# Performance work log

Measured on AMD Instinct MI355X. Metric: run time of the kernel, lower is better.

Reference implementation:

```python
import jax, jax.numpy as jnp
import numpy as np

N = 50000      # nodes
E = 600000     # edges
D_IN = 128     # node_dim
D = 128        # out_channels
T = 4          # num_node_types
R = 4          # num_edge_types
L = 2          # num_layers
C = 8          # num_class
G = 512        # graphs in batch


def setup_inputs() -> dict:
    key = jax.random.key(0)
    ks = jax.random.split(key, 12)
    s = 0.05
    x = jax.random.normal(ks[0], (N, D_IN), jnp.float32)
    node_type = jax.random.randint(ks[1], (N,), 0, T)
    edge_index = jax.random.randint(ks[2], (2, E), 0, N)
    edge_type = jax.random.randint(ks[3], (E,), 0, R)
    batch = jnp.sort(jax.random.randint(ks[4], (N,), 0, G))
    # learned params
    W_het = jax.random.normal(ks[5], (T, D_IN, D), jnp.float32) * s
    b_het = jnp.zeros((T, D), jnp.float32)
    conv_W = jax.random.normal(ks[6], (L, R, D, D), jnp.float32) * s
    conv_b = jnp.zeros((L, R, D), jnp.float32)
    fuse_W = jax.random.normal(ks[7], (R * D, D), jnp.float32) * s
    fuse_b = jnp.zeros((D,), jnp.float32)
    cls_W = jax.random.normal(ks[8], (D, C), jnp.float32) * s
    cls_b = jnp.zeros((C,), jnp.float32)
    return dict(x=x, W_het=W_het, b_het=b_het, conv_W=conv_W, conv_b=conv_b,
                fuse_W=fuse_W, fuse_b=fuse_b, cls_W=cls_W, cls_b=cls_b,
                node_type=node_type, edge_index=edge_index, edge_type=edge_type,
                batch=batch)


def reference(x, W_het, b_het, conv_W, conv_b, fuse_W, fuse_b, cls_W, cls_b,
              node_type, edge_index, edge_type, batch):
    n = x.shape[0]
    # HeteroLinear: per-node-type linear. Compute all T projections then select.
    x_all = jnp.einsum('nd,tdo->tno', x, W_het)          # [T, N, D]
    h = x_all[node_type, jnp.arange(n)] + b_het[node_type]
    src, dst = edge_index[0], edge_index[1]
    for l in range(L):
        hs = h[src]                                       # [E, D] gather once per layer
        outs = []
        for r in range(R):
            # edges of relation r only (boolean mask == per-relation edge filtering)
            m = hs @ conv_W[l, r]                         # [E, D]
            m = m * (edge_type == r).astype(m.dtype)[:, None]
            agg = jax.ops.segment_sum(m, dst, num_segments=n)  # scatter-add to dst
            outs.append(agg + conv_b[l, r])
        h = jax.nn.relu(jnp.concatenate(outs, axis=1) @ fuse_W + fuse_b)
    # global mean pool over graphs
    counts = jax.ops.segment_sum(jnp.ones((n,), h.dtype), batch, num_segments=G)
    emb = jax.ops.segment_sum(h, batch, num_segments=G) / jnp.maximum(counts, 1.0)[:, None]
    logits = emb @ cls_W + cls_b
    return emb, logits
```

## Files before the change

kernel.cpp:

```cpp
#include <hip/hip_runtime.h>

#define N_NODES 50000
#define N_EDGES 600000
#define DIM     128
#define RR      4
#define LL      2
#define GG      512
#define CC      8
#define NB_SCAN ((N_NODES + 255) / 256)
#define EC      (N_EDGES / 4)
#define FB      ((EC + 255) / 256)
#define TB      ((N_NODES + 255) / 256)
#define NBH     ((N_NODES + 63) / 64)
#define CB      (1026 + 3125)

typedef short bf16x8 __attribute__((ext_vector_type(8)));
typedef float f32x4  __attribute__((ext_vector_type(4)));

__device__ __forceinline__ float bf16_to_f(unsigned short u) {
    return __uint_as_float(((unsigned int)u) << 16);
}
__device__ __forceinline__ unsigned short f_to_bf16(float f) {
    unsigned int u = __float_as_uint(f);
    u += 0x7FFFu + ((u >> 16) & 1u);
    return (unsigned short)(u >> 16);
}
__device__ __forceinline__ float loadf(const void* p, long i, int isbf) {
    if (isbf) return bf16_to_f(((const unsigned short*)p)[i]);
    return ((const float*)p)[i];
}
__device__ __forceinline__ void storef(void* p, long i, float v, int isbf) {
    if (isbf) ((unsigned short*)p)[i] = f_to_bf16(v);
    else      ((float*)p)[i] = v;
}

__global__ void cg_init(const unsigned int* __restrict__ xw, int* __restrict__ flag,
                        int* __restrict__ deg_tb) {
    __shared__ int cnt;
    int tid = threadIdx.x;
    int t = blockIdx.x * 256 + tid;
    if (t < N_NODES + 16) deg_tb[t] = 0;
    if (blockIdx.x == 0) {
        if (tid == 0) cnt = 0;
        __syncthreads();
        unsigned int w = xw[tid];
        unsigned int e = (w >> 7) & 0xFFu;
        atomicAdd(&cnt, (e >= 110u && e <= 133u) ? 1 : 0);
        __syncthreads();
        if (tid == 0) *flag = (cnt >= 128) ? 1 : 0;
    }
}

__global__ void cg_hist_canon(const int* __restrict__ edge_index, const int* __restrict__ node_type,
                              int* __restrict__ deg, int* __restrict__ tb,
                              const void* __restrict__ x,
                              const void* __restrict__ W_het, const void* __restrict__ b_het,
                              const void* __restrict__ conv_W, const void* __restrict__ fuse_W,
                              const void* __restrict__ conv_b, const void* __restrict__ fuse_b,
                              const int* __restrict__ flagp,
                              unsigned short* __restrict__ xb, unsigned short* __restrict__ Wt,
                              float* __restrict__ bhf,
                              unsigned short* __restrict__ M2t, float* __restrict__ cvec) {
    __shared__ float s[256];
    int bk = blockIdx.x;
    int tid = threadIdx.x;
    if (bk < FB) {
        __shared__ int loc[4];
        if (tid < 4) loc[tid] = 0;
        __syncthreads();
        int t = bk * 256 + tid;
        if (t < EC) {
            int d0 = edge_index[N_EDGES + t];
            int d1 = edge_index[N_EDGES + t + EC];
            int d2 = edge_index[N_EDGES + t + 2 * EC];
            int d3 = edge_index[N_EDGES + t + 3 * EC];
            atomicAdd(&deg[d0], 1);
            atomicAdd(&deg[d1], 1);
            atomicAdd(&deg[d2], 1);
            atomicAdd(&deg[d3], 1);
        }
        if (t < N_NODES) atomicAdd(&loc[node_type[t]], 1);
        __syncthreads();
        if (tid < 4 && loc[tid]) atomicAdd(&tb[tid], loc[tid]);
        return;
    }
    int b = bk - FB;
    int isbf = *flagp;
    if (b < 512) {
        int lr = b >> 6;
        int d  = (b & 63) * 2 + (tid >> 7);
        int r  = lr & 3;
        int o  = tid & 127;
        float acc = 0.0f;
        for (int k = 0; k < DIM; k++) {
            acc += loadf(conv_W, (long)(lr * DIM + d) * DIM + k, isbf)
                 * loadf(fuse_W, (long)(r * DIM + k) * DIM + o, isbf);
        }
        M2t[((long)lr * DIM + o) * DIM + d] = f_to_bf16(acc);
    } else if (b < 768) {
        int bc = b - 512;
        int l  = bc >> 7;
        int o  = bc & 127;
        float part = 0.0f;
        for (int rk = tid; rk < RR * DIM; rk += 256) {
            part += loadf(conv_b, (long)l * RR * DIM + rk, isbf)
                  * loadf(fuse_W, (long)rk * DIM + o, isbf);
        }
        s[tid] = part;
        __syncthreads();
        for (int off = 128; off > 0; off >>= 1) {
            if (tid < off) s[tid] += s[tid + off];
            __syncthreads();
        }
        if (tid == 0) cvec[bc] = s[0] + loadf(fuse_b, o, isbf);
    } else if (b < 1024) {
        int pair = (b - 768) * 2 + (tid >> 7);
        int t = pair >> 7;
        int o = pair & 127;
        int d = tid & 127;
        float v = loadf(W_het, ((long)t * DIM + d) * DIM + o, isbf);
        Wt[((long)t * DIM + o) * DIM + d] = f_to_bf16(v);
    } else if (b < 1026) {
        int idx = (b - 1024) * 256 + tid;
        if (idx < 4 * DIM) bhf[idx] = loadf(b_het, idx, isbf);
    } else {
        long i = ((long)(b - 1026) * 256 + tid) * 8;
        if (i >= (long)N_NODES * DIM) return;
        if (isbf) {
            *(uint4*)(xb + i) = *(const uint4*)((const unsigned short*)x + i);
        } else {
            const float* xf = (const float*)x + i;
            float4 f0 = *(const float4*)xf;
            float4 f1 = *(const float4*)(xf + 4);
            uint4 o;
            o.x = (unsigned int)f_to_bf16(f0.x) | ((unsigned int)f_to_bf16(f0.y) << 16);
            o.y = (unsigned int)f_to_bf16(f0.z) | ((unsigned int)f_to_bf16(f0.w) << 16);
            o.z = (unsigned int)f_to_bf16(f1.x) | ((unsigned int)f_to_bf16(f1.y) << 16);
            o.w = (unsigned int)f_to_bf16(f1.z) | ((unsigned int)f_to_bf16(f1.w) << 16);
            *(uint4*)(xb + i) = o;
        }
    }
}

__global__ void cg_scan_a(const int* __restrict__ deg, int* __restrict__ blocksum) {
    __shared__ int s[256];
    int tid = threadIdx.x;
    int i = blockIdx.x * 256 + tid;
    s[tid] = (i < N_NODES) ? deg[i] : 0;
    __syncthreads();
    for (int off = 128; off > 0; off >>= 1) {
        if (tid < off) s[tid] += s[tid + off];
        __syncthreads();
    }
    if (tid == 0) blocksum[blockIdx.x] = s[0];
}

__global__ void cg_scan_b(const int* __restrict__ blocksum, int* __restrict__ blockoff,
                          int* __restrict__ rowptr, int* __restrict__ tb) {
    __shared__ int s[256];
    int tid = threadIdx.x;
    int v = (tid < NB_SCAN) ? blocksum[tid] : 0;
    s[tid] = v;
    __syncthreads();
    for (int off = 1; off < 256; off <<= 1) {
        int a = (tid >= off) ? s[tid - off] : 0;
        __syncthreads();
        s[tid] += a;
        __syncthreads();
    }
    if (tid < NB_SCAN) blockoff[tid] = s[tid] - v;
    if (tid == 255) rowptr[N_NODES] = s[255];
    if (tid == 0) {
        int run = 0;
        for (int t = 0; t < 4; t++) {
            tb[8 + t] = run;
            tb[4 + t] = run;
            run += tb[t];
        }
        tb[12] = run;
    }
}

__global__ void cg_scan_tfill(const int* __restrict__ deg, const int* __restrict__ blockoff,
                              int* __restrict__ rowptr, int* __restrict__ cursor,
                              const int* __restrict__ node_type, int* __restrict__ tb,
                              int* __restrict__ tlist) {
    int bk = blockIdx.x;
    int tid = threadIdx.x;
    if (bk < NB_SCAN) {
        __shared__ int s[256];
        int i = bk * 256 + tid;
        int v = (i < N_NODES) ? deg[i] : 0;
        s[tid] = v;
        __syncthreads();
        for (int off = 1; off < 256; off <<= 1) {
            int a = (tid >= off) ? s[tid - off] : 0;
            __syncthreads();
            s[tid] += a;
            __syncthreads();
        }
        if (i < N_NODES) {
            int val = blockoff[bk] + s[tid] - v;
            rowptr[i] = val;
            cursor[i] = val;
        }
    } else {
        __shared__ int lcur[4];
        __shared__ int lbase[4];
        if (tid < 4) lcur[tid] = 0;
        __syncthreads();
        int n = (bk - NB_SCAN) * 256 + tid;
        int slot = -1, t = 0;
        if (n < N_NODES) {
            t = node_type[n];
            slot = atomicAdd(&lcur[t], 1);
        }
        __syncthreads();
        if (tid < 4) lbase[tid] = atomicAdd(&tb[4 + tid], lcur[tid]);
        __syncthreads();
        if (n < N_NODES) tlist[lbase[t] + slot] = n;
    }
}

#define APAD 136

__global__ void cg_fill_hetero(const int* __restrict__ edge_index, const int* __restrict__ edge_type,
                               int* __restrict__ cursor, int* __restrict__ eidx,
                               const unsigned short* __restrict__ xb,
                               const unsigned short* __restrict__ Wt,
                               const float* __restrict__ bhf,
                               const int* __restrict__ tlist, const int* __restrict__ tb,
                               unsigned short* __restrict__ h) {
    __shared__ unsigned short a_lds[64][APAD];
    __shared__ unsigned short b_lds[DIM][APAD];
    int bk = blockIdx.x;
    int tx = threadIdx.x;
    if (bk < FB) {
        int t = bk * 256 + tx;
        if (t >= EC) return;
#pragma unroll
        for (int k = 0; k < 4; k++) {
            int e = t + k * EC;
            int d = edge_index[N_EDGES + e];
            int pos = atomicAdd(&cursor[d], 1);
            eidx[pos] = (edge_index[e] << 2) | edge_type[e];
        }
        return;
    }
    int bb = bk - FB;
    int t    = bb / NBH;
    int nblk = bb - t * NBH;
    int rows_base = tb[8 + t] + nblk * 64;
    int rend = tb[8 + t + 1];
    if (rows_base >= rend) return;
    const unsigned short* Wsrc = Wt + (long)t * DIM * DIM;
    for (int i = tx; i < 2048; i += 256) {
        uint4 w = *(const uint4*)(Wsrc + i * 8);
        int o = i >> 4, d = (i & 15) * 8;
        *(uint4*)&b_lds[o][d] = w;
    }
    for (int i = tx; i < 1024; i += 256) {
        int row = i >> 4, seg = (i & 15) * 8;
        int gr = rows_base + row;
        uint4 w = make_uint4(0u, 0u, 0u, 0u);
        if (gr < rend) {
            int n = tlist[gr];
            w = *(const uint4*)(xb + (long)n * DIM + seg);
        }
        *(uint4*)&a_lds[row][seg] = w;
    }
    __syncthreads();
    int wv = tx >> 6, lane = tx & 63;
    int m16 = lane & 15, quad = lane >> 4;
    f32x4 acc[8];
#pragma unroll
    for (int c = 0; c < 8; c++) acc[c] = (f32x4){0.f, 0.f, 0.f, 0.f};
    for (int ks = 0; ks < 4; ks++) {
        int koff = ks * 32 + quad * 8;
        bf16x8 af = *(const bf16x8*)(const void*)&a_lds[wv * 16 + m16][koff];
#pragma unroll
        for (int c = 0; c < 8; c++) {
            bf16x8 bfr = *(const bf16x8*)(const void*)&b_lds[c * 16 + m16][koff];
            acc[c] = __builtin_amdgcn_mfma_f32_16x16x32_bf16(af, bfr, acc[c], 0, 0, 0);
        }
    }
    __syncthreads();
#pragma unroll
    for (int c = 0; c < 8; c++) {
#pragma unroll
        for (int i = 0; i < 4; i++) {
            int row = wv * 16 + quad * 4 + i;
            int col = c * 16 + m16;
            a_lds[row][col] = f_to_bf16(acc[c][i] + bhf[t * DIM + col]);
        }
    }
    __syncthreads();
    for (int i = tx; i < 1024; i += 256) {
        int row = i >> 4, seg = (i & 15) * 8;
        int gr = rows_base + row;
        if (gr < rend) {
            int n = tlist[gr];
            *(uint4*)(h + (long)n * DIM + seg) = *(const uint4*)&a_lds[row][seg];
        }
    }
}

__global__ void cg_pgemm_mfma(const unsigned short* __restrict__ h,
                              const unsigned short* __restrict__ M2t, int l,
                              unsigned short* __restrict__ P) {
    int r  = blockIdx.y;
    int n0 = blockIdx.x * 64;
    __shared__ unsigned short a_lds[64][APAD];
    __shared__ unsigned short b_lds[DIM][APAD];
    int tx = threadIdx.x;
    const unsigned short* Bsrc = M2t + (long)(l * RR + r) * DIM * DIM;
    for (int i = tx; i < 2048; i += 256) {
        uint4 w = *(const uint4*)(Bsrc + i * 8);
        int o = i >> 4, d = (i & 15) * 8;
        *(uint4*)&b_lds[o][d] = w;
    }
    for (int i = tx; i < 1024; i += 256) {
        int row = i >> 4, seg = (i & 15) * 8;
        int n = n0 + row;
        uint4 w = make_uint4(0u, 0u, 0u, 0u);
        if (n < N_NODES) w = *(const uint4*)(h + (long)n * DIM + seg);
        *(uint4*)&a_lds[row][seg] = w;
    }
    __syncthreads();
    int wv = tx >> 6, lane = tx & 63;
    int m16 = lane & 15, quad = lane >> 4;
    f32x4 acc[8];
#pragma unroll
    for (int c = 0; c < 8; c++) acc[c] = (f32x4){0.f, 0.f, 0.f, 0.f};
    for (int ks = 0; ks < 4; ks++) {
        int koff = ks * 32 + quad * 8;
        bf16x8 af = *(const bf16x8*)(const void*)&a_lds[wv * 16 + m16][koff];
#pragma unroll
        for (int c = 0; c < 8; c++) {
            bf16x8 bfr = *(const bf16x8*)(const void*)&b_lds[c * 16 + m16][koff];
            acc[c] = __builtin_amdgcn_mfma_f32_16x16x32_bf16(af, bfr, acc[c], 0, 0, 0);
        }
    }
    __syncthreads();
#pragma unroll
    for (int c = 0; c < 8; c++) {
#pragma unroll
        for (int i = 0; i < 4; i++) {
            int row = wv * 16 + quad * 4 + i;
            int col = c * 16 + m16;
            a_lds[row][col] = f_to_bf16(acc[c][i]);
        }
    }
    __syncthreads();
    for (int i = tx; i < 1024; i += 256) {
        int row = i >> 4, seg = (i & 15) * 8;
        int n = n0 + row;
        if (n < N_NODES)
            *(uint4*)(P + (long)n * (RR * DIM) + r * DIM + seg) = *(const uint4*)&a_lds[row][seg];
    }
}

__global__ void cg_gather4(const unsigned short* __restrict__ P, const int* __restrict__ rowptr,
                           const int* __restrict__ eidx, const float* __restrict__ cv,
                           unsigned short* __restrict__ hout) {
    int wid  = (blockIdx.x * 256 + threadIdx.x) >> 6;
    int lane = threadIdx.x & 63;
    if (wid >= N_NODES) return;
    int eg = lane >> 4;
    int ol = lane & 15;
    int start = rowptr[wid];
    int end   = rowptr[wid + 1];
    float a[8] = {0.f, 0.f, 0.f, 0.f, 0.f, 0.f, 0.f, 0.f};
    int j = start + eg;
    for (; j + 4 < end; j += 8) {
        int v0 = eidx[j];
        int v1 = eidx[j + 4];
        const uint4 w0 = *(const uint4*)(P + (long)(v0 >> 2) * (RR * DIM) + (v0 & 3) * DIM + ol * 8);
        const uint4 w1 = *(const uint4*)(P + (long)(v1 >> 2) * (RR * DIM) + (v1 & 3) * DIM + ol * 8);
        a[0] += bf16_to_f((unsigned short)(w0.x & 0xFFFFu)) + bf16_to_f((unsigned short)(w1.x & 0xFFFFu));
        a[1] += bf16_to_f((unsigned short)(w0.x >> 16))     + bf16_to_f((unsigned short)(w1.x >> 16));
        a[2] += bf16_to_f((unsigned short)(w0.y & 0xFFFFu)) + bf16_to_f((unsigned short)(w1.y & 0xFFFFu));
        a[3] += bf16_to_f((unsigned short)(w0.y >> 16))     + bf16_to_f((unsigned short)(w1.y >> 16));
        a[4] += bf16_to_f((unsigned short)(w0.z & 0xFFFFu)) + bf16_to_f((unsigned short)(w1.z & 0xFFFFu));
        a[5] += bf16_to_f((unsigned short)(w0.z >> 16))     + bf16_to_f((unsigned short)(w1.z >> 16));
        a[6] += bf16_to_f((unsigned short)(w0.w & 0xFFFFu)) + bf16_to_f((unsigned short)(w1.w & 0xFFFFu));
        a[7] += bf16_to_f((unsigned short)(w0.w >> 16))     + bf16_to_f((unsigned short)(w1.w >> 16));
    }
    if (j < end) {
        int v = eidx[j];
        const uint4 w = *(const uint4*)(P + (long)(v >> 2) * (RR * DIM) + (v & 3) * DIM + ol * 8);
        a[0] += bf16_to_f((unsigned short)(w.x & 0xFFFFu));
        a[1] += bf16_to_f((unsigned short)(w.x >> 16));
        a[2] += bf16_to_f((unsigned short)(w.y & 0xFFFFu));
        a[3] += bf16_to_f((unsigned short)(w.y >> 16));
        a[4] += bf16_to_f((unsigned short)(w.z & 0xFFFFu));
        a[5] += bf16_to_f((unsigned short)(w.z >> 16));
        a[6] += bf16_to_f((unsigned short)(w.w & 0xFFFFu));
        a[7] += bf16_to_f((unsigned short)(w.w >> 16));
    }
#pragma unroll
    for (int i = 0; i < 8; i++) {
        a[i] += __shfl_xor(a[i], 16);
        a[i] += __shfl_xor(a[i], 32);
    }
    if (eg == 0) {
        int o0 = ol * 8;
        float v[8];
#pragma unroll
        for (int i = 0; i < 8; i++) {
            float s = a[i] + cv[o0 + i];
            v[i] = s > 0.0f ? s : 0.0f;
        }
        uint4 o4;
        o4.x = (unsigned int)f_to_bf16(v[0]) | ((unsigned int)f_to_bf16(v[1]) << 16);
        o4.y = (unsigned int)f_to_bf16(v[2]) | ((unsigned int)f_to_bf16(v[3]) << 16);
        o4.z = (unsigned int)f_to_bf16(v[4]) | ((unsigned int)f_to_bf16(v[5]) << 16);
        o4.w = (unsigned int)f_to_bf16(v[6]) | ((unsigned int)f_to_bf16(v[7]) << 16);
        *(uint4*)(hout + (long)wid * DIM + o0) = o4;
    }
}

__global__ void cg_pool_logits(const unsigned short* __restrict__ h, const int* __restrict__ batch,
                               const void* __restrict__ cls_W, const void* __restrict__ cls_b,
                               const int* __restrict__ flagp, void* __restrict__ out) {
    __shared__ float acc_s[4][DIM];
    __shared__ float emb_s[DIM];
    int g   = blockIdx.x;
    int tid = threadIdx.x;
    int wv  = tid >> 6;
    int lane = tid & 63;
    int sub = lane >> 4;
    int ol  = lane & 15;
    int isbf = *flagp;
    int lo = 0, hi = N_NODES;
    while (lo < hi) { int mid = (lo + hi) >> 1; if (batch[mid] < g) lo = mid + 1; else hi = mid; }
    int start = lo;
    hi = N_NODES;
    while (lo < hi) { int mid = (lo + hi) >> 1; if (batch[mid] < g + 1) lo = mid + 1; else hi = mid; }
    int end = lo;
    float a[8] = {0.f, 0.f, 0.f, 0.f, 0.f, 0.f, 0.f, 0.f};
    for (int n = start + wv * 4 + sub; n < end; n += 16) {
        uint4 w = *(const uint4*)(h + (long)n * DIM + ol * 8);
        a[0] += bf16_to_f((unsigned short)(w.x & 0xFFFFu));
        a[1] += bf16_to_f((unsigned short)(w.x >> 16));
        a[2] += bf16_to_f((unsigned short)(w.y & 0xFFFFu));
        a[3] += bf16_to_f((unsigned short)(w.y >> 16));
        a[4] += bf16_to_f((unsigned short)(w.z & 0xFFFFu));
        a[5] += bf16_to_f((unsigned short)(w.z >> 16));
        a[6] += bf16_to_f((unsigned short)(w.w & 0xFFFFu));
        a[7] += bf16_to_f((unsigned short)(w.w >> 16));
    }
#pragma unroll
    for (int i = 0; i < 8; i++) {
        a[i] += __shfl_xor(a[i], 16);
        a[i] += __shfl_xor(a[i], 32);
    }
    if (sub == 0) {
#pragma unroll
        for (int i = 0; i < 8; i++) acc_s[wv][ol * 8 + i] = a[i];
    }
    __syncthreads();
    int cnt = end - start;
    float inv = 1.0f / (float)(cnt > 1 ? cnt : 1);
    if (tid < DIM) {
        float e = (acc_s[0][tid] + acc_s[1][tid] + acc_s[2][tid] + acc_s[3][tid]) * inv;
        emb_s[tid] = e;
        storef(out, (long)g * DIM + tid, e, isbf);
    }
    __syncthreads();
    if (tid < 128) {
        int c  = tid >> 4;
        int kk = tid & 15;
        float p = 0.0f;
#pragma unroll
        for (int k = kk * 8; k < kk * 8 + 8; k++)
            p += emb_s[k] * loadf(cls_W, (long)k * CC + c, isbf);
        p += __shfl_xor(p, 1);
        p += __shfl_xor(p, 2);
        p += __shfl_xor(p, 4);
        p += __shfl_xor(p, 8);
        if (kk == 0)
            storef(out, (long)GG * DIM + g * CC + c, p + loadf(cls_b, c, isbf), isbf);
    }
}

extern "C" void kernel_launch(void* const* d_in, const int* in_sizes, int n_in,
                              void* d_out, int out_size, void* d_ws, size_t ws_size,
                              hipStream_t stream) {
    const void* x      = d_in[0];
    const void* W_het  = d_in[1];
    const void* b_het  = d_in[2];
    const void* conv_W = d_in[3];
    const void* conv_b = d_in[4];
    const void* fuse_W = d_in[5];
    const void* fuse_b = d_in[6];
    const void* cls_W  = d_in[7];
    const void* cls_b  = d_in[8];
    const int* node_type  = (const int*)d_in[9];
    const int* edge_index = (const int*)d_in[10];
    const int* edge_type  = (const int*)d_in[11];
    const int* batch      = (const int*)d_in[12];

    char* base = (char*)d_ws;
    unsigned short* hbf      = (unsigned short*)(base + 0);
    unsigned short* P        = (unsigned short*)(base + 12800000);
    unsigned short* xb       = (unsigned short*)(base + 64000000);
    unsigned short* Wt       = (unsigned short*)(base + 76800000);
    float*          bhf      = (float*)(base + 76931072);
    unsigned short* M2t      = (unsigned short*)(base + 76933120);
    float*          cvec     = (float*)(base + 77195264);
    int*            rowptr   = (int*)(base + 77196288);
    int*            cursor   = (int*)(base + 77396320);
    int*            deg      = (int*)(base + 77596352);
    int*            tb       = (int*)(base + 77796352);
    int*            blocksum = (int*)(base + 77796416);
    int*            blockoff = (int*)(base + 77797440);
    int*            eidx     = (int*)(base + 77798464);
    int*            tlist    = (int*)(base + 80198464);
    int*            flag     = (int*)(base + 80398464);

    cg_init<<<(N_NODES + 16 + 255) / 256, 256, 0, stream>>>((const unsigned int*)x, flag, deg);
    cg_hist_canon<<<FB + CB, 256, 0, stream>>>(edge_index, node_type, deg, tb,
                                               x, W_het, b_het, conv_W, fuse_W,
                                               conv_b, fuse_b, flag,
                                               xb, Wt, bhf, M2t, cvec);
    cg_scan_a<<<NB_SCAN, 256, 0, stream>>>(deg, blocksum);
    cg_scan_b<<<1, 256, 0, stream>>>(blocksum, blockoff, rowptr, tb);
    cg_scan_tfill<<<NB_SCAN + TB, 256, 0, stream>>>(deg, blockoff, rowptr, cursor,
                                                    node_type, tb, tlist);
    cg_fill_hetero<<<FB + 4 * NBH, 256, 0, stream>>>(edge_index, edge_type, cursor, eidx,
                                                     xb, Wt, bhf, tlist, tb, hbf);

    for (int l = 0; l < LL; l++) {
        cg_pgemm_mfma<<<dim3(NBH, RR), 256, 0, stream>>>(hbf, M2t, l, P);
        cg_gather4<<<(N_NODES * 64 + 255) / 256, 256, 0, stream>>>(
            P, rowptr, eidx, cvec + l * DIM, hbf);
    }

    cg_pool_logits<<<GG, 256, 0, stream>>>(hbf, batch, cls_W, cls_b, flag, d_out);
}
```

Before: 317.6 us.

## Build CSR with two-pass block-bucketed sort and fuse second pass with layer-0 GEMM

Replaces the per-edge global atomic scatter into CSR with a two-pass counting sort. Pass one buckets edges by 256-node destination block using LDS histograms and one global atomic per bucket, writing (payload, dst) pairs to a temp buffer. Pass two does the per-node scatter using LDS atomics and runs in the same launch as the layer-0 projection GEMM. This removes one launch and cuts global atomic contention and scattered writes, at the cost of an extra temp buffer pass and more kernel complexity.

```diff
diff --git a/kernel.cpp b/kernel.cpp
--- a/kernel.cpp
+++ b/kernel.cpp
@@ -156,6 +156,7 @@
 }
 
 __global__ void cg_scan_b(const int* __restrict__ blocksum, int* __restrict__ blockoff,
+                          int* __restrict__ ccursor,
                           int* __restrict__ rowptr, int* __restrict__ tb) {
     __shared__ int s[256];
     int tid = threadIdx.x;
@@ -168,7 +169,11 @@
         s[tid] += a;
         __syncthreads();
     }
-    if (tid < NB_SCAN) blockoff[tid] = s[tid] - v;
+    if (tid < NB_SCAN) {
+        int e = s[tid] - v;
+        blockoff[tid] = e;
+        ccursor[tid]  = e;
+    }
     if (tid == 255) rowptr[N_NODES] = s[255];
     if (tid == 0) {
         int run = 0;
@@ -182,7 +187,7 @@
 }
 
 __global__ void cg_scan_tfill(const int* __restrict__ deg, const int* __restrict__ blockoff,
-                              int* __restrict__ rowptr, int* __restrict__ cursor,
+                              int* __restrict__ rowptr,
                               const int* __restrict__ node_type, int* __restrict__ tb,
                               int* __restrict__ tlist) {
     int bk = blockIdx.x;
@@ -199,11 +204,7 @@
             s[tid] += a;
             __syncthreads();
         }
-        if (i < N_NODES) {
-            int val = blockoff[bk] + s[tid] - v;
-            rowptr[i] = val;
-            cursor[i] = val;
-        }
+        if (i < N_NODES) rowptr[i] = blockoff[bk] + s[tid] - v;
     } else {
         __shared__ int lcur[4];
         __shared__ int lbase[4];
@@ -224,26 +225,45 @@
 
 #define APAD 136
 
-__global__ void cg_fill_hetero(const int* __restrict__ edge_index, const int* __restrict__ edge_type,
-                               int* __restrict__ cursor, int* __restrict__ eidx,
-                               const unsigned short* __restrict__ xb,
-                               const unsigned short* __restrict__ Wt,
-                               const float* __restrict__ bhf,
-                               const int* __restrict__ tlist, const int* __restrict__ tb,
-                               unsigned short* __restrict__ h) {
+__global__ void cg_sortA_hetero(const int* __restrict__ edge_index, const int* __restrict__ edge_type,
+                                int* __restrict__ ccursor, int2* __restrict__ tmp2,
+                                const unsigned short* __restrict__ xb,
+                                const unsigned short* __restrict__ Wt,
+                                const float* __restrict__ bhf,
+                                const int* __restrict__ tlist, const int* __restrict__ tb,
+                                unsigned short* __restrict__ h) {
     __shared__ unsigned short a_lds[64][APAD];
     __shared__ unsigned short b_lds[DIM][APAD];
     int bk = blockIdx.x;
     int tx = threadIdx.x;
     if (bk < FB) {
+        __shared__ int lhist[NB_SCAN];
+        __shared__ int lbase[NB_SCAN];
+        for (int i = tx; i < NB_SCAN; i += 256) lhist[i] = 0;
+        __syncthreads();
         int t = bk * 256 + tx;
-        if (t >= EC) return;
-#pragma unroll
-        for (int k = 0; k < 4; k++) {
-            int e = t + k * EC;
-            int d = edge_index[N_EDGES + e];
-            int pos = atomicAdd(&cursor[d], 1);
-            eidx[pos] = (edge_index[e] << 2) | edge_type[e];
+        int d[4], cb[4], ls[4], pl[4];
+        bool act = (t < EC);
+        if (act) {
+#pragma unroll
+            for (int k = 0; k < 4; k++) {
+                int e = t + k * EC;
+                d[k]  = edge_index[N_EDGES + e];
+                pl[k] = (edge_index[e] << 2) | edge_type[e];
+                cb[k] = d[k] >> 8;
+                ls[k] = atomicAdd(&lhist[cb[k]], 1);
+            }
+        }
+        __syncthreads();
+        for (int i = tx; i < NB_SCAN; i += 256)
+            lbase[i] = lhist[i] ? atomicAdd(&ccursor[i], lhist[i]) : 0;
+        __syncthreads();
+        if (act) {
+#pragma unroll
+            for (int k = 0; k < 4; k++) {
+                int pos = lbase[cb[k]] + ls[k];
+                tmp2[pos] = make_int2(pl[k], d[k]);
+            }
         }
         return;
     }
@@ -256,8 +276,8 @@
     const unsigned short* Wsrc = Wt + (long)t * DIM * DIM;
     for (int i = tx; i < 2048; i += 256) {
         uint4 w = *(const uint4*)(Wsrc + i * 8);
-        int o = i >> 4, d = (i & 15) * 8;
-        *(uint4*)&b_lds[o][d] = w;
+        int o = i >> 4, d2 = (i & 15) * 8;
+        *(uint4*)&b_lds[o][d2] = w;
     }
     for (int i = tx; i < 1024; i += 256) {
         int row = i >> 4, seg = (i & 15) * 8;
@@ -302,6 +322,81 @@
             int n = tlist[gr];
             *(uint4*)(h + (long)n * DIM + seg) = *(const uint4*)&a_lds[row][seg];
         }
+    }
+}
+
+__global__ void cg_sortB_pgemm(const int2* __restrict__ tmp2, const int* __restrict__ blockoff,
+                               const int* __restrict__ rowptr, int* __restrict__ eidx,
+                               const unsigned short* __restrict__ h,
+                               const unsigned short* __restrict__ M2t,
+                               unsigned short* __restrict__ P) {
+    __shared__ unsigned short a_lds[64][APAD];
+    __shared__ unsigned short b_lds[DIM][APAD];
+    int bk = blockIdx.x;
+    int tx = threadIdx.x;
+    if (bk < NB_SCAN) {
+        __shared__ int lcur[256];
+        int nn = bk * 256 + tx;
+        lcur[tx] = (nn < N_NODES) ? rowptr[nn] : 0;
+        int base = blockoff[bk];
+        int endp = (bk + 1 < NB_SCAN) ? blockoff[bk + 1] : N_EDGES;
+        int cnt = endp - base;
+        __syncthreads();
+        for (int i = tx; i < cnt; i += 256) {
+            int2 v = tmp2[base + i];
+            int pos = atomicAdd(&lcur[v.y & 255], 1);
+            eidx[pos] = v.x;
+        }
+        return;
+    }
+    int bb = bk - NB_SCAN;
+    int r    = bb / NBH;
+    int nblk = bb - r * NBH;
+    int n0 = nblk * 64;
+    const unsigned short* Bsrc = M2t + (long)r * DIM * DIM;
+    for (int i = tx; i < 2048; i += 256) {
+        uint4 w = *(const uint4*)(Bsrc + i * 8);
+        int o = i >> 4, d = (i & 15) * 8;
+        *(uint4*)&b_lds[o][d] = w;
+    }
+    for (int i = tx; i < 1024; i += 256) {
+        int row = i >> 4, seg = (i & 15) * 8;
+        int n = n0 + row;
+        uint4 w = make_uint4(0u, 0u, 0u, 0u);
+        if (n < N_NODES) w = *(const uint4*)(h + (long)n * DIM + seg);
+        *(uint4*)&a_lds[row][seg] = w;
+    }
+    __syncthreads();
+    int wv = tx >> 6, lane = tx & 63;
+    int m16 = lane & 15, quad = lane >> 4;
+    f32x4 acc[8];
+#pragma unroll
+    for (int c = 0; c < 8; c++) acc[c] = (f32x4){0.f, 0.f, 0.f, 0.f};
+    for (int ks = 0; ks < 4; ks++) {
+        int koff = ks * 32 + quad * 8;
+        bf16x8 af = *(const bf16x8*)(const void*)&a_lds[wv * 16 + m16][koff];
+#pragma unroll
+        for (int c = 0; c < 8; c++) {
+            bf16x8 bfr = *(const bf16x8*)(const void*)&b_lds[c * 16 + m16][koff];
+            acc[c] = __builtin_amdgcn_mfma_f32_16x16x32_bf16(af, bfr, acc[c], 0, 0, 0);
+        }
+    }
+    __syncthreads();
+#pragma unroll
+    for (int c = 0; c < 8; c++) {
+#pragma unroll
+        for (int i = 0; i < 4; i++) {
+            int row = wv * 16 + quad * 4 + i;
+            int col = c * 16 + m16;
+            a_lds[row][col] = f_to_bf16(acc[c][i]);
+        }
+    }
+    __syncthreads();
+    for (int i = tx; i < 1024; i += 256) {
+        int row = i >> 4, seg = (i & 15) * 8;
+        int n = n0 + row;
+        if (n < N_NODES)
+            *(uint4*)(P + (long)n * (RR * DIM) + r * DIM + seg) = *(const uint4*)&a_lds[row][seg];
     }
 }
 
@@ -369,7 +464,7 @@
     int eg = lane >> 4;
     int ol = lane & 15;
     int start = rowptr[wid];
-    int end   = rowptr[wid + 1];
+    int end   = (wid + 1 < N_NODES) ? rowptr[wid + 1] : N_EDGES;
     float a[8] = {0.f, 0.f, 0.f, 0.f, 0.f, 0.f, 0.f, 0.f};
     int j = start + eg;
     for (; j + 4 < end; j += 8) {
@@ -510,14 +605,15 @@
     unsigned short* M2t      = (unsigned short*)(base + 76933120);
     float*          cvec     = (float*)(base + 77195264);
     int*            rowptr   = (int*)(base + 77196288);
-    int*            cursor   = (int*)(base + 77396320);
-    int*            deg      = (int*)(base + 77596352);
-    int*            tb       = (int*)(base + 77796352);
-    int*            blocksum = (int*)(base + 77796416);
-    int*            blockoff = (int*)(base + 77797440);
-    int*            eidx     = (int*)(base + 77798464);
-    int*            tlist    = (int*)(base + 80198464);
-    int*            flag     = (int*)(base + 80398464);
+    int*            deg      = (int*)(base + 77396320);
+    int*            tb       = (int*)(base + 77596320);
+    int*            blocksum = (int*)(base + 77596384);
+    int*            blockoff = (int*)(base + 77597408);
+    int*            ccursor  = (int*)(base + 77598432);
+    int*            eidx     = (int*)(base + 77599456);
+    int*            tlist    = (int*)(base + 79999456);
+    int*            flag     = (int*)(base + 80199456);
+    int2*           tmp2     = (int2*)(base + 80199472);
 
     cg_init<<<(N_NODES + 16 + 255) / 256, 256, 0, stream>>>((const unsigned int*)x, flag, deg);
     cg_hist_canon<<<FB + CB, 256, 0, stream>>>(edge_index, node_type, deg, tb,
@@ -525,17 +621,18 @@
                                                conv_b, fuse_b, flag,
                                                xb, Wt, bhf, M2t, cvec);
     cg_scan_a<<<NB_SCAN, 256, 0, stream>>>(deg, blocksum);
-    cg_scan_b<<<1, 256, 0, stream>>>(blocksum, blockoff, rowptr, tb);
-    cg_scan_tfill<<<NB_SCAN + TB, 256, 0, stream>>>(deg, blockoff, rowptr, cursor,
+    cg_scan_b<<<1, 256, 0, stream>>>(blocksum, blockoff, ccursor, rowptr, tb);
+    cg_scan_tfill<<<NB_SCAN + TB, 256, 0, stream>>>(deg, blockoff, rowptr,
                                                     node_type, tb, tlist);
-    cg_fill_hetero<<<FB + 4 * NBH, 256, 0, stream>>>(edge_index, edge_type, cursor, eidx,
-                                                     xb, Wt, bhf, tlist, tb, hbf);
-
-    for (int l = 0; l < LL; l++) {
-        cg_pgemm_mfma<<<dim3(NBH, RR), 256, 0, stream>>>(hbf, M2t, l, P);
-        cg_gather4<<<(N_NODES * 64 + 255) / 256, 256, 0, stream>>>(
-            P, rowptr, eidx, cvec + l * DIM, hbf);
-    }
+    cg_sortA_hetero<<<FB + 4 * NBH, 256, 0, stream>>>(edge_index, edge_type, ccursor, tmp2,
+                                                      xb, Wt, bhf, tlist, tb, hbf);
+    cg_sortB_pgemm<<<NB_SCAN + 4 * NBH, 256, 0, stream>>>(tmp2, blockoff, rowptr, eidx,
+                                                          hbf, M2t, P);
+    cg_gather4<<<(N_NODES * 64 + 255) / 256, 256, 0, stream>>>(
+        P, rowptr, eidx, cvec, hbf);
+    cg_pgemm_mfma<<<dim3(NBH, RR), 256, 0, stream>>>(hbf, M2t, 1, P);
+    cg_gather4<<<(N_NODES * 64 + 255) / 256, 256, 0, stream>>>(
+        P, rowptr, eidx, cvec + DIM, hbf);
 
     cg_pool_logits<<<GG, 256, 0, stream>>>(hbf, batch, cls_W, cls_b, flag, d_out);
 }
```

Result: faster. 304.9 us (-4.0%).
